# Performance work log

Hardware: AMD Instinct MI355X
Metric: run time of the kernel (lower is better)

Reference implementation:

```python
import jax, jax.numpy as jnp
import numpy as np

D_MODEL = 1024; N_HEAD = 16; HD = 64
D_STATE = 128; D_CONV = 4; EXPAND = 2; HEADDIM = 64
D_INNER = EXPAND * D_MODEL          # 2048
NHEADS = D_INNER // HEADDIM         # 32
FFN = 4 * D_MODEL                   # 4096
B, T = 2, 1024


def rmsnorm(x, eps=1e-6):
    # FastSimpleRMSNorm: no learnable weight
    return x * jax.lax.rsqrt(jnp.mean(x * x, axis=-1, keepdims=True) + eps)


def causal_dwconv(x, w, b):
    # x: (..., T, C), w: (C, K), b: (C,). Causal depthwise conv (left pad K-1).
    K = w.shape[1]
    t = x.shape[-2]
    pad = [(0, 0)] * (x.ndim - 2) + [(K - 1, 0), (0, 0)]
    xp = jnp.pad(x, pad)
    y = jnp.zeros_like(x) + b
    for k in range(K):
        y = y + w[:, k] * jax.lax.slice_in_dim(xp, k, k + t, axis=-2)
    return y


def block_forward(x, W_in, conv_w, conv_b, A_log, Dm, dt_bias, mnorm_w, W_out,
                  W_qkv, W_cproj, qconv_w, qconv_b, kconv_w, kconv_b, vconv_w, vconv_b,
                  time_maa_k, time_maa_r, W_key, W_rec, W_val):
    Bsz, Tn, _ = x.shape
    # ---- Mamba2 branch ----
    h = rmsnorm(x)
    zxbcdt = h @ W_in                                  # (B,T,2*D_INNER+2*N+H)
    z = zxbcdt[..., :D_INNER]
    xBC = zxbcdt[..., D_INNER:2 * D_INNER + 2 * D_STATE]
    dt = zxbcdt[..., -NHEADS:]
    xBC = jax.nn.silu(causal_dwconv(xBC, conv_w, conv_b))
    xm = xBC[..., :D_INNER]
    Bm = xBC[..., D_INNER:D_INNER + D_STATE]           # (B,T,N)
    Cm = xBC[..., -D_STATE:]                           # (B,T,N)
    dt = jax.nn.softplus(dt + dt_bias)                 # (B,T,H)
    A = -jnp.exp(A_log)                                # (H,)
    xh = xm.reshape(Bsz, Tn, NHEADS, HEADDIM)          # (B,T,H,P)

    def step(hstate, inp):
        dt_t, x_t, B_t, C_t = inp                      # (B,H),(B,H,P),(B,N),(B,N)
        dA = jnp.exp(dt_t * A)                         # (B,H)
        hstate = hstate * dA[..., None, None] + (dt_t[..., None] * x_t)[..., None] * B_t[:, None, None, :]
        y_t = jnp.einsum('bhpn,bn->bhp', hstate, C_t)
        return hstate, y_t

    h0 = jnp.zeros((Bsz, NHEADS, HEADDIM, D_STATE), x.dtype)
    _, ys = jax.lax.scan(step, h0, (jnp.swapaxes(dt, 0, 1), jnp.swapaxes(xh, 0, 1),
                                    jnp.swapaxes(Bm, 0, 1), jnp.swapaxes(Cm, 0, 1)))
    y = jnp.swapaxes(ys, 0, 1) + xh * Dm[:, None]      # (B,T,H,P)
    y = y.reshape(Bsz, Tn, D_INNER) * jax.nn.silu(z)   # gated
    y = y * jax.lax.rsqrt(jnp.mean(y * y, axis=-1, keepdims=True) + 1e-5) * mnorm_w
    x = x + y @ W_out

    # ---- MQA with depthwise convs ----
    h = rmsnorm(x)
    qkv = h @ W_qkv                                    # (B,T,D_MODEL+2*HD)
    q = qkv[..., :D_MODEL].reshape(Bsz, Tn, N_HEAD, HD).transpose(0, 2, 1, 3)  # (B,H,T,D)
    k = qkv[..., D_MODEL:D_MODEL + HD]                 # (B,T,D) single kv head
    v = qkv[..., -HD:]
    q = causal_dwconv(q, qconv_w, qconv_b)
    k = causal_dwconv(k, kconv_w, kconv_b)
    v = causal_dwconv(v, vconv_w, vconv_b)
    scores = jnp.einsum('bhtd,bsd->bhts', q, k) / np.float32(np.sqrt(HD))
    mask = jnp.tril(jnp.ones((Tn, Tn), bool))
    scores = jnp.where(mask, scores, -jnp.inf)
    p = jax.nn.softmax(scores, axis=-1)
    y = jnp.einsum('bhts,bsd->bhtd', p, v)
    y = y.transpose(0, 2, 1, 3).reshape(Bsz, Tn, D_MODEL)
    x = x + y @ W_cproj

    # ---- RWKV CMix FFN ----
    h = rmsnorm(x)
    xx = jnp.pad(h, ((0, 0), (1, 0), (0, 0)))[:, :Tn] - h   # time_shift(x) - x
    xk = h + xx * time_maa_k
    xr = h + xx * time_maa_r
    kf = jnp.square(jax.nn.relu(xk @ W_key))           # ReLU^2
    kv = kf @ W_val
    x = x + jax.nn.sigmoid(xr @ W_rec) * kv
    return x


def setup_inputs() -> dict:
    key = jax.random.key(0)
    ks = jax.random.split(key, 16)
    def w(k, shape, sc=0.02):
        return jax.random.normal(k, shape, jnp.float32) * sc
    x = jax.random.normal(ks[0], (B, T, D_MODEL), jnp.float32)
    W_in = w(ks[1], (D_MODEL, 2 * D_INNER + 2 * D_STATE + NHEADS))
    conv_w = w(ks[2], (D_INNER + 2 * D_STATE, D_CONV), 0.2)
    conv_b = jnp.zeros((D_INNER + 2 * D_STATE,), jnp.float32)
    A_log = jnp.log(jnp.arange(1, NHEADS + 1, dtype=jnp.float32))
    Dm = jnp.ones((NHEADS,), jnp.float32)
    dt_bias = w(ks[3], (NHEADS,), 0.5)
    mnorm_w = jnp.ones((D_INNER,), jnp.float32)
    W_out = w(ks[4], (D_INNER, D_MODEL))
    W_qkv = w(ks[5], (D_MODEL, D_MODEL + 2 * HD))
    W_cproj = w(ks[6], (D_MODEL, D_MODEL))
    qconv_w = w(ks[7], (HD, 3), 0.3); qconv_b = jnp.zeros((HD,), jnp.float32)
    kconv_w = w(ks[8], (HD, 3), 0.3); kconv_b = jnp.zeros((HD,), jnp.float32)
    vconv_w = w(ks[9], (HD, 3), 0.3); vconv_b = jnp.zeros((HD,), jnp.float32)
    ddd = jnp.arange(D_MODEL, dtype=jnp.float32) / D_MODEL
    time_maa_k = 1.0 - ddd  # layer_id=0 -> ratio_1_to_almost0 = 1
    time_maa_r = 1.0 - ddd
    W_key = w(ks[10], (D_MODEL, FFN))
    W_rec = w(ks[11], (D_MODEL, D_MODEL))
    W_val = w(ks[12], (FFN, D_MODEL))
    return dict(x=x, W_in=W_in, conv_w=conv_w, conv_b=conv_b, A_log=A_log, Dm=Dm,
                dt_bias=dt_bias, mnorm_w=mnorm_w, W_out=W_out, W_qkv=W_qkv, W_cproj=W_cproj,
                qconv_w=qconv_w, qconv_b=qconv_b, kconv_w=kconv_w, kconv_b=kconv_b,
                vconv_w=vconv_w, vconv_b=vconv_b, time_maa_k=time_maa_k, time_maa_r=time_maa_r,
                W_key=W_key, W_rec=W_rec, W_val=W_val)


def reference(x, W_in, conv_w, conv_b, A_log, Dm, dt_bias, mnorm_w, W_out,
              W_qkv, W_cproj, qconv_w, qconv_b, kconv_w, kconv_b, vconv_w, vconv_b,
              time_maa_k, time_maa_r, W_key, W_rec, W_val):
    return block_forward(x, W_in, conv_w, conv_b, A_log, Dm, dt_bias, mnorm_w, W_out,
                         W_qkv, W_cproj, qconv_w, qconv_b, kconv_w, kconv_b, vconv_w, vconv_b,
                         time_maa_k, time_maa_r, W_key, W_rec, W_val)
```

## Files before the change

### kernel.cpp

```cpp
#include <hip/hip_runtime.h>
#include <hip/hip_bf16.h>
#include <math.h>

#define BB 2
#define TT 1024
#define BT (BB*TT)
#define DM 1024
#define DI 2048
#define DS 128
#define NHS 32
#define PDIM 64
#define NHA 16
#define HD 64
#define FFN_ 4096
#define NZX 4384
#define NXBC 2304
#define NXBCD 2336
#define CL 128
#define NC 8

typedef __hip_bfloat16 bf16;
typedef short bf16x8 __attribute__((ext_vector_type(8)));
typedef float f32x4 __attribute__((ext_vector_type(4)));

__device__ __forceinline__ float b2f(bf16 v){ return __bfloat162float(v); }
__device__ __forceinline__ bf16 f2b(float v){ return __float2bfloat16(v); }

__device__ __forceinline__ void gload16(const void* g, void* l) {
  __builtin_amdgcn_global_load_lds(
      (const __attribute__((address_space(1))) unsigned int*)g,
      (__attribute__((address_space(3))) unsigned int*)l,
      16, 0, 0);
}

__global__ void k_rms_in(const float* __restrict__ xin, float* __restrict__ X,
                         bf16* __restrict__ H) {
  int row = blockIdx.x;
  int tid = threadIdx.x;
  const float* xr = xin + (size_t)row * DM;
  float v[4]; float ss = 0.f;
  #pragma unroll
  for (int i = 0; i < 4; ++i) { v[i] = xr[tid*4+i]; ss += v[i]*v[i]; }
  __shared__ float red[256];
  red[tid] = ss; __syncthreads();
  for (int s = 128; s > 0; s >>= 1) { if (tid < s) red[tid] += red[tid+s]; __syncthreads(); }
  float scale = rsqrtf(red[0]/(float)DM + 1e-6f);
  float* Xr = X + (size_t)row*DM; bf16* Hr = H + (size_t)row*DM;
  #pragma unroll
  for (int i = 0; i < 4; ++i) { Xr[tid*4+i] = v[i]; Hr[tid*4+i] = f2b(v[i]*scale); }
}

__global__ void k_reduce4_rms(const float* __restrict__ p0, const float* __restrict__ p1,
                              const float* __restrict__ p2, const float* __restrict__ p3,
                              float* __restrict__ X, bf16* __restrict__ H) {
  int row = blockIdx.x; int tid = threadIdx.x;
  size_t base = (size_t)row*DM + tid*4;
  float4 a = *(const float4*)(p0 + base);
  float4 b = *(const float4*)(p1 + base);
  float4 c = *(const float4*)(p2 + base);
  float4 d = *(const float4*)(p3 + base);
  float4 x = *(const float4*)(X + base);
  float v[4];
  v[0] = x.x + a.x + b.x + c.x + d.x;
  v[1] = x.y + a.y + b.y + c.y + d.y;
  v[2] = x.z + a.z + b.z + c.z + d.z;
  v[3] = x.w + a.w + b.w + c.w + d.w;
  float ss = v[0]*v[0] + v[1]*v[1] + v[2]*v[2] + v[3]*v[3];
  __shared__ float red[256];
  red[tid] = ss; __syncthreads();
  for (int s = 128; s > 0; s >>= 1) { if (tid < s) red[tid] += red[tid+s]; __syncthreads(); }
  float scale = rsqrtf(red[0]/(float)DM + 1e-6f);
  float4 res; res.x = v[0]; res.y = v[1]; res.z = v[2]; res.w = v[3];
  *(float4*)(X + base) = res;
  bf16* Hr = H + (size_t)row*DM + tid*4;
  #pragma unroll
  for (int i = 0; i < 4; ++i) Hr[i] = f2b(v[i]*scale);
}

__global__ void k_rms_shift(const float* __restrict__ X, const float* __restrict__ maak,
                            const float* __restrict__ maar,
                            bf16* __restrict__ XK, bf16* __restrict__ XR) {
  int row = blockIdx.x; int t = row & (TT - 1);
  int tid = threadIdx.x;
  const float* xr = X + (size_t)row*DM;
  const float* xp = xr - DM;
  float v[4], pv[4]; float ss = 0.f, ssp = 0.f;
  #pragma unroll
  for (int i = 0; i < 4; ++i) {
    int c = tid*4 + i;
    v[i] = xr[c]; ss += v[i]*v[i];
    pv[i] = (t > 0) ? xp[c] : 0.f; ssp += pv[i]*pv[i];
  }
  __shared__ float red[256], red2[256];
  red[tid] = ss; red2[tid] = ssp; __syncthreads();
  for (int s = 128; s > 0; s >>= 1) {
    if (tid < s) { red[tid] += red[tid+s]; red2[tid] += red2[tid+s]; }
    __syncthreads();
  }
  float scale  = rsqrtf(red[0]/(float)DM + 1e-6f);
  float scalep = (t > 0) ? rsqrtf(red2[0]/(float)DM + 1e-6f) : 0.f;
  bf16* xk = XK + (size_t)row*DM; bf16* xrw = XR + (size_t)row*DM;
  #pragma unroll
  for (int i = 0; i < 4; ++i) {
    int c = tid*4 + i;
    float h = v[i]*scale;
    float xx = pv[i]*scalep - h;
    xk[c]  = f2b(h + xx*maak[c]);
    xrw[c] = f2b(h + xx*maar[c]);
  }
}

__global__ void k_tcast(const float* __restrict__ W, bf16* __restrict__ Wt,
                        int K, int N) {
  __shared__ float t[32][33];
  int tx = threadIdx.x, ty = threadIdx.y;
  int n0 = blockIdx.x*32, k0 = blockIdx.y*32;
  #pragma unroll
  for (int i = 0; i < 4; ++i) {
    int k = k0 + ty + i*8, n = n0 + tx;
    t[ty + i*8][tx] = (n < N) ? W[(size_t)k*N + n] : 0.f;
  }
  __syncthreads();
  #pragma unroll
  for (int i = 0; i < 4; ++i) {
    int n = n0 + ty + i*8, k = k0 + tx;
    Wt[(size_t)n*K + k] = f2b(t[tx][ty + i*8]);
  }
}

template<int EPI, bool ADD, bool OUTBF>
__global__ __launch_bounds__(256)
void mfma_gemm(const bf16* __restrict__ A, const bf16* __restrict__ Bt,
               float* __restrict__ C, bf16* __restrict__ Cbf,
               int M, int N, int K) {
  __shared__ bf16 As[128*32];
  __shared__ bf16 Bs[128*32];
  int tid = threadIdx.x;
  int wave = tid >> 6, lane = tid & 63;
  int m_l = lane & 15, quad = lane >> 4;
  int wr = (wave & 1) * 64, wc = (wave >> 1) * 64;
  int row0 = blockIdx.y * 128, col0 = blockIdx.x * 128;
  f32x4 acc[4][4];
  #pragma unroll
  for (int i = 0; i < 4; ++i)
    #pragma unroll
    for (int j = 0; j < 4; ++j) acc[i][j] = (f32x4){0.f,0.f,0.f,0.f};
  int lr = lane >> 2;
  int lc = (lane & 3) * 8;
  for (int k0 = 0; k0 < K; k0 += 32) {
    __syncthreads();
    #pragma unroll
    for (int g = 0; g < 2; ++g) {
      int rbase = 32*wave + 16*g;
      gload16(&A [(size_t)(row0 + rbase + lr)*K + k0 + lc], &As[rbase*32]);
      gload16(&Bt[(size_t)(col0 + rbase + lr)*K + k0 + lc], &Bs[rbase*32]);
    }
    __syncthreads();
    bf16x8 af[4], bfv[4];
    #pragma unroll
    for (int i = 0; i < 4; ++i) af[i]  = *(const bf16x8*)&As[(wr + i*16 + m_l)*32 + quad*8];
    #pragma unroll
    for (int j = 0; j < 4; ++j) bfv[j] = *(const bf16x8*)&Bs[(wc + j*16 + m_l)*32 + quad*8];
    #pragma unroll
    for (int i = 0; i < 4; ++i)
      #pragma unroll
      for (int j = 0; j < 4; ++j)
        acc[i][j] = __builtin_amdgcn_mfma_f32_16x16x32_bf16(af[i], bfv[j], acc[i][j], 0, 0, 0);
  }
  #pragma unroll
  for (int i = 0; i < 4; ++i) {
    #pragma unroll
    for (int j = 0; j < 4; ++j) {
      int col = col0 + wc + j*16 + m_l;
      if (col < N) {
        #pragma unroll
        for (int r = 0; r < 4; ++r) {
          int row = row0 + wr + i*16 + quad*4 + r;
          float v = acc[i][j][r];
          if (EPI == 1) { v = fmaxf(v, 0.f); v = v*v; }
          else if (EPI == 2) v = 1.f/(1.f + __expf(-v));
          if (OUTBF)      Cbf[(size_t)row*N + col] = f2b(v);
          else if (ADD)   C[(size_t)row*N + col] += v;
          else            C[(size_t)row*N + col]  = v;
        }
      }
    }
  }
}

__global__ __launch_bounds__(256)
void mfma_sk32(const bf16* __restrict__ A, const bf16* __restrict__ Bt,
               float* __restrict__ P0, float* __restrict__ P1,
               float* __restrict__ P2, float* __restrict__ P3,
               int M, int N, int K, int kchunk) {
  __shared__ bf16 As[128*32];
  __shared__ bf16 Bs[128*32];
  int tid = threadIdx.x;
  int wave = tid >> 6, lane = tid & 63;
  int m_l = lane & 15, quad = lane >> 4;
  int wr = (wave & 1) * 64, wc = (wave >> 1) * 64;
  int row0 = blockIdx.y * 128, col0 = blockIdx.x * 128;
  int kbeg = blockIdx.z * kchunk;
  int kend = kbeg + kchunk;
  f32x4 acc[4][4];
  #pragma unroll
  for (int i = 0; i < 4; ++i)
    #pragma unroll
    for (int j = 0; j < 4; ++j) acc[i][j] = (f32x4){0.f,0.f,0.f,0.f};
  int lr = lane >> 2;
  int lc = (lane & 3) * 8;
  for (int k0 = kbeg; k0 < kend; k0 += 32) {
    __syncthreads();
    #pragma unroll
    for (int g = 0; g < 2; ++g) {
      int rbase = 32*wave + 16*g;
      gload16(&A [(size_t)(row0 + rbase + lr)*K + k0 + lc], &As[rbase*32]);
      gload16(&Bt[(size_t)(col0 + rbase + lr)*K + k0 + lc], &Bs[rbase*32]);
    }
    __syncthreads();
    bf16x8 af[4], bfv[4];
    #pragma unroll
    for (int i = 0; i < 4; ++i) af[i]  = *(const bf16x8*)&As[(wr + i*16 + m_l)*32 + quad*8];
    #pragma unroll
    for (int j = 0; j < 4; ++j) bfv[j] = *(const bf16x8*)&Bs[(wc + j*16 + m_l)*32 + quad*8];
    #pragma unroll
    for (int i = 0; i < 4; ++i)
      #pragma unroll
      for (int j = 0; j < 4; ++j)
        acc[i][j] = __builtin_amdgcn_mfma_f32_16x16x32_bf16(af[i], bfv[j], acc[i][j], 0, 0, 0);
  }
  float* P = (blockIdx.z == 0) ? P0 : (blockIdx.z == 1) ? P1 : (blockIdx.z == 2) ? P2 : P3;
  #pragma unroll
  for (int i = 0; i < 4; ++i) {
    #pragma unroll
    for (int j = 0; j < 4; ++j) {
      int col = col0 + wc + j*16 + m_l;
      if (col < N) {
        #pragma unroll
        for (int r = 0; r < 4; ++r) {
          int row = row0 + wr + i*16 + quad*4 + r;
          P[(size_t)row*N + col] = acc[i][j][r];
        }
      }
    }
  }
}

template<int Z, int EPI, bool ADD>
__global__ void k_reduce(float* __restrict__ dst, const float* __restrict__ p0,
                         const float* __restrict__ p1, const float* __restrict__ p2,
                         const float* __restrict__ p3) {
  size_t i = ((size_t)blockIdx.x*256 + threadIdx.x)*4;
  float4 a = *(const float4*)(p0 + i);
  float4 b = *(const float4*)(p1 + i);
  float r0 = a.x + b.x, r1 = a.y + b.y, r2 = a.z + b.z, r3 = a.w + b.w;
  if (Z == 4) {
    float4 c = *(const float4*)(p2 + i);
    float4 d = *(const float4*)(p3 + i);
    r0 += c.x + d.x; r1 += c.y + d.y; r2 += c.z + d.z; r3 += c.w + d.w;
  }
  if (EPI == 2) {
    r0 = 1.f/(1.f + __expf(-r0)); r1 = 1.f/(1.f + __expf(-r1));
    r2 = 1.f/(1.f + __expf(-r2)); r3 = 1.f/(1.f + __expf(-r3));
  }
  if (ADD) {
    float4 o = *(const float4*)(dst + i);
    r0 += o.x; r1 += o.y; r2 += o.z; r3 += o.w;
  }
  float4 res; res.x = r0; res.y = r1; res.z = r2; res.w = r3;
  *(float4*)(dst + i) = res;
}

__global__ void k_reduce_final6(const float* __restrict__ k0, const float* __restrict__ k1,
                                const float* __restrict__ k2, const float* __restrict__ k3,
                                const float* __restrict__ r0p, const float* __restrict__ r1p,
                                const float* __restrict__ X, float* __restrict__ out) {
  size_t i = ((size_t)blockIdx.x*256 + threadIdx.x)*4;
  float4 a = *(const float4*)(k0 + i);
  float4 b = *(const float4*)(k1 + i);
  float4 c = *(const float4*)(k2 + i);
  float4 d = *(const float4*)(k3 + i);
  float4 ra = *(const float4*)(r0p + i);
  float4 rb = *(const float4*)(r1p + i);
  float4 x = *(const float4*)(X + i);
  float kvx = a.x + b.x + c.x + d.x, kvy = a.y + b.y + c.y + d.y;
  float kvz = a.z + b.z + c.z + d.z, kvw = a.w + b.w + c.w + d.w;
  float sx = 1.f/(1.f + __expf(-(ra.x + rb.x)));
  float sy = 1.f/(1.f + __expf(-(ra.y + rb.y)));
  float sz = 1.f/(1.f + __expf(-(ra.z + rb.z)));
  float sw = 1.f/(1.f + __expf(-(ra.w + rb.w)));
  float4 res;
  res.x = x.x + sx*kvx; res.y = x.y + sy*kvy;
  res.z = x.z + sz*kvz; res.w = x.w + sw*kvw;
  *(float4*)(out + i) = res;
}

__global__ void k_conv_ssm(const float* __restrict__ ZXr, const float* __restrict__ cw,
                           const float* __restrict__ cb, const float* __restrict__ dtb,
                           bf16* __restrict__ XBCb, float* __restrict__ DT) {
  int bt = blockIdx.x; int b = bt >> 10; int t = bt & 1023;
  int tid = threadIdx.x;
  for (int c = tid; c < NXBC; c += 256) {
    float acc = cb[c];
    #pragma unroll
    for (int kk = 0; kk < 4; ++kk) {
      int ts = t - 3 + kk;
      if (ts >= 0) acc += cw[c*4+kk] * ZXr[((size_t)(b*TT+ts))*NXBCD + c];
    }
    float s = acc / (1.f + __expf(-acc));
    XBCb[(size_t)bt*NXBC + c] = f2b(s);
  }
  if (tid < NHS) {
    float x = ZXr[(size_t)bt*NXBCD + NXBC + tid] + dtb[tid];
    float sp = (x > 20.f) ? x : log1pf(__expf(x));
    DT[(size_t)bt*NHS + tid] = sp;
  }
}

__global__ __launch_bounds__(512)
void k_scan1(const bf16* __restrict__ xbcb, const float* __restrict__ dt,
             const float* __restrict__ A_log, const float* __restrict__ Dmv,
             float* __restrict__ Y, float* __restrict__ SC, float* __restrict__ CUM) {
  int bc = blockIdx.x;
  int bh = bc >> 3, c = bc & 7;
  int b = bh >> 5, h = bh & 31;
  int tid = threadIdx.x, wave = tid >> 6, lane = tid & 63;
  int col = lane & 15, quad = lane >> 4;
  int t0 = c * CL;
  __shared__ bf16 sB[128*136];
  __shared__ bf16 sC[128*136];
  __shared__ bf16 sxT[64*136];
  __shared__ float sL[128], sdt[128], sW[128];
  float A = -__expf(A_log[h]);
  float Dmh = Dmv[h];
  for (int e = tid; e < 128*16; e += 512) {
    int r = e >> 4, ch = e & 15;
    const bf16* row = xbcb + (size_t)(b*TT + t0 + r)*NXBC;
    *(uint4*)&sB[r*136 + ch*8] = *(const uint4*)&row[2048 + ch*8];
    *(uint4*)&sC[r*136 + ch*8] = *(const uint4*)&row[2176 + ch*8];
  }
  for (int e = tid; e < 64*128; e += 512) {
    int p = e & 63, t = e >> 6;
    sxT[p*136 + t] = xbcb[(size_t)(b*TT + t0 + t)*NXBC + h*64 + p];
  }
  if (tid < 128) sdt[tid] = dt[(size_t)(b*TT + t0 + tid)*NHS + h];
  __syncthreads();
  if (wave == 0) {
    float a0 = sdt[2*lane]*A, a1 = sdt[2*lane+1]*A;
    float tot = a0 + a1;
    #pragma unroll
    for (int off = 1; off < 64; off <<= 1) {
      float up = __shfl_up(tot, off);
      if (lane >= off) tot += up;
    }
    sL[2*lane+1] = tot;
    sL[2*lane]   = tot - a1;
  }
  __syncthreads();
  int wr = (wave & 1)*64, wc = (wave >> 1)*32;
  f32x4 g[4][2];
  #pragma unroll
  for (int i = 0; i < 4; ++i)
    #pragma unroll
    for (int j = 0; j < 2; ++j) g[i][j] = (f32x4){0.f,0.f,0.f,0.f};
  #pragma unroll
  for (int kf = 0; kf < 4; ++kf) {
    bf16x8 af[4], bfr[2];
    #pragma unroll
    for (int i = 0; i < 4; ++i) af[i]  = *(const bf16x8*)&sC[(wr + i*16 + col)*136 + kf*32 + quad*8];
    #pragma unroll
    for (int j = 0; j < 2; ++j) bfr[j] = *(const bf16x8*)&sB[(wc + j*16 + col)*136 + kf*32 + quad*8];
    #pragma unroll
    for (int i = 0; i < 4; ++i)
      #pragma unroll
      for (int j = 0; j < 2; ++j)
        g[i][j] = __builtin_amdgcn_mfma_f32_16x16x32_bf16(af[i], bfr[j], g[i][j], 0, 0, 0);
  }
  float Lend = sL[127];
  if (tid < 128) sW[tid] = __expf(Lend - sL[tid]) * sdt[tid];
  __syncthreads();
  if (tid < 128) CUM[(size_t)bh*TT + t0 + tid] = __expf(sL[tid]);
  #pragma unroll
  for (int i = 0; i < 4; ++i) {
    #pragma unroll
    for (int j = 0; j < 2; ++j) {
      int sl = wc + j*16 + col;
      #pragma unroll
      for (int r = 0; r < 4; ++r) {
        int tl = wr + i*16 + quad*4 + r;
        float v = (sl <= tl) ? g[i][j][r] * __expf(sL[tl] - sL[sl]) * sdt[sl] : 0.f;
        sC[tl*136 + sl] = f2b(v);
      }
    }
  }
  for (int e = tid; e < 128*128; e += 512) {
    int n = e & 127, s = e >> 7;
    sB[n*136 + s] = f2b(b2f(xbcb[(size_t)(b*TT + t0 + s)*NXBC + 2048 + n]) * sW[s]);
  }
  __syncthreads();
  int tb = (wave & 3)*32, pb = (wave >> 2)*32;
  f32x4 ya[2][2];
  #pragma unroll
  for (int i2 = 0; i2 < 2; ++i2)
    #pragma unroll
    for (int jd = 0; jd < 2; ++jd) ya[i2][jd] = (f32x4){0.f,0.f,0.f,0.f};
  #pragma unroll
  for (int kf = 0; kf < 4; ++kf) {
    bf16x8 pa[2], xa[2];
    #pragma unroll
    for (int i2 = 0; i2 < 2; ++i2)
      pa[i2] = *(const bf16x8*)&sC[(tb + i2*16 + col)*136 + kf*32 + quad*8];
    #pragma unroll
    for (int jd = 0; jd < 2; ++jd)
      xa[jd] = *(const bf16x8*)&sxT[(pb + jd*16 + col)*136 + kf*32 + quad*8];
    #pragma unroll
    for (int i2 = 0; i2 < 2; ++i2)
      #pragma unroll
      for (int jd = 0; jd < 2; ++jd)
        ya[i2][jd] = __builtin_amdgcn_mfma_f32_16x16x32_bf16(pa[i2], xa[jd], ya[i2][jd], 0, 0, 0);
  }
  #pragma unroll
  for (int i2 = 0; i2 < 2; ++i2) {
    #pragma unroll
    for (int jd = 0; jd < 2; ++jd) {
      int p = pb + jd*16 + col;
      #pragma unroll
      for (int r = 0; r < 4; ++r) {
        int tl = tb + i2*16 + quad*4 + r;
        float xv = b2f(sxT[p*136 + tl]);
        Y[(size_t)(b*TT + t0 + tl)*DI + h*64 + p] = ya[i2][jd][r] + xv*Dmh;
      }
    }
  }
  int pb3 = (wave & 3)*16, nb = (wave >> 2)*64;
  f32x4 sa[4];
  #pragma unroll
  for (int nt = 0; nt < 4; ++nt) sa[nt] = (f32x4){0.f,0.f,0.f,0.f};
  #pragma unroll
  for (int kf = 0; kf < 4; ++kf) {
    bf16x8 xpa = *(const bf16x8*)&sxT[(pb3 + col)*136 + kf*32 + quad*8];
    #pragma unroll
    for (int nt = 0; nt < 4; ++nt) {
      bf16x8 bwa = *(const bf16x8*)&sB[(nb + nt*16 + col)*136 + kf*32 + quad*8];
      sa[nt] = __builtin_amdgcn_mfma_f32_16x16x32_bf16(xpa, bwa, sa[nt], 0, 0, 0);
    }
  }
  #pragma unroll
  for (int nt = 0; nt < 4; ++nt) {
    int n = nb + nt*16 + col;
    #pragma unroll
    for (int r = 0; r < 4; ++r) {
      int p = pb3 + quad*4 + r;
      SC[((size_t)(bh*NC + c)*64 + p)*128 + n] = sa[nt][r];
    }
  }
}

__global__ __launch_bounds__(512)
void k_scan2(float* __restrict__ SC, const float* __restrict__ CUM) {
  int bh = blockIdx.x;
  int tid = threadIdx.x;
  int p = tid >> 3, g = tid & 7;
  float S[16];
  #pragma unroll
  for (int j = 0; j < 16; ++j) S[j] = 0.f;
  for (int c = 0; c < NC; ++c) {
    size_t base = ((size_t)(bh*NC + c)*64 + p)*128 + g*16;
    float Ptot = CUM[(size_t)bh*TT + c*CL + (CL-1)];
    float tmp[16];
    #pragma unroll
    for (int j = 0; j < 16; ++j) tmp[j] = SC[base + j];
    #pragma unroll
    for (int j = 0; j < 16; ++j) SC[base + j] = S[j];
    #pragma unroll
    for (int j = 0; j < 16; ++j) S[j] = S[j]*Ptot + tmp[j];
  }
}

__global__ __launch_bounds__(256)
void k_scan3(const bf16* __restrict__ xbcb, const float* __restrict__ SC,
             const float* __restrict__ CUM, float* __restrict__ Y) {
  int bc = blockIdx.x;
  int bh = bc >> 3, c = bc & 7;
  if (c == 0) return;
  int b = bh >> 5, h = bh & 31;
  int tid = threadIdx.x, wave = tid >> 6, lane = tid & 63;
  int col = lane & 15, quad = lane >> 4;
  int t0 = c * CL;
  __shared__ bf16 sCt[128*136];
  __shared__ bf16 sS[64*136];
  __shared__ float sCum[128];
  for (int e = tid; e < 128*16; e += 256) {
    int r = e >> 4, ch = e & 15;
    *(uint4*)&sCt[r*136 + ch*8] =
      *(const uint4*)&xbcb[(size_t)(b*TT + t0 + r)*NXBC + 2176 + ch*8];
  }
  for (int e = tid; e < 64*128; e += 256) {
    int n = e & 127, p = e >> 7;
    sS[p*136 + n] = f2b(SC[((size_t)(bh*NC + c)*64 + p)*128 + n]);
  }
  if (tid < 128) sCum[tid] = CUM[(size_t)bh*TT + t0 + tid];
  __syncthreads();
  f32x4 ya[2][4];
  #pragma unroll
  for (int i2 = 0; i2 < 2; ++i2)
    #pragma unroll
    for (int jd = 0; jd < 4; ++jd) ya[i2][jd] = (f32x4){0.f,0.f,0.f,0.f};
  #pragma unroll
  for (int kf = 0; kf < 4; ++kf) {
    bf16x8 pa[2], sv[4];
    #pragma unroll
    for (int i2 = 0; i2 < 2; ++i2)
      pa[i2] = *(const bf16x8*)&sCt[(wave*32 + i2*16 + col)*136 + kf*32 + quad*8];
    #pragma unroll
    for (int jd = 0; jd < 4; ++jd)
      sv[jd] = *(const bf16x8*)&sS[(jd*16 + col)*136 + kf*32 + quad*8];
    #pragma unroll
    for (int i2 = 0; i2 < 2; ++i2)
      #pragma unroll
      for (int jd = 0; jd < 4; ++jd)
        ya[i2][jd] = __builtin_amdgcn_mfma_f32_16x16x32_bf16(pa[i2], sv[jd], ya[i2][jd], 0, 0, 0);
  }
  #pragma unroll
  for (int i2 = 0; i2 < 2; ++i2) {
    #pragma unroll
    for (int jd = 0; jd < 4; ++jd) {
      int p = jd*16 + col;
      #pragma unroll
      for (int r = 0; r < 4; ++r) {
        int tl = wave*32 + i2*16 + quad*4 + r;
        Y[(size_t)(b*TT + t0 + tl)*DI + h*64 + p] += sCum[tl]*ya[i2][jd][r];
      }
    }
  }
}

__global__ void k_gate(const float* __restrict__ Y, const float* __restrict__ Z,
                       const float* __restrict__ mnw, bf16* __restrict__ Ybf) {
  int row = blockIdx.x; int tid = threadIdx.x;
  const float* yr = Y + (size_t)row*DI;
  const float* zr = Z + (size_t)row*DI;
  float gv[8]; float ss = 0.f;
  #pragma unroll
  for (int i = 0; i < 8; ++i) {
    int c = tid*8 + i;
    float z = zr[c];
    float sz = z / (1.f + __expf(-z));
    float v = yr[c]*sz;
    gv[i] = v; ss += v*v;
  }
  __shared__ float red[256];
  red[tid] = ss; __syncthreads();
  for (int s = 128; s > 0; s >>= 1) { if (tid < s) red[tid] += red[tid+s]; __syncthreads(); }
  float scale = rsqrtf(red[0]/(float)DI + 1e-5f);
  bf16* br = Ybf + (size_t)row*DI;
  #pragma unroll
  for (int i = 0; i < 8; ++i) { int c = tid*8 + i; br[c] = f2b(gv[i]*scale*mnw[c]); }
}

__global__ void k_conv_qkv(const float* __restrict__ QKV,
                           const float* qw, const float* qb, const float* kw, const float* kb,
                           const float* vw, const float* vb,
                           bf16* __restrict__ Qb, bf16* __restrict__ Kb, bf16* __restrict__ Vtb) {
  int bt = blockIdx.x; int b = bt >> 10; int t = bt & 1023;
  int tid = threadIdx.x;
  for (int c = tid; c < 1152; c += 256) {
    if (c < 1024) {
      int h = c >> 6, d = c & 63;
      float acc = qb[d];
      #pragma unroll
      for (int kk = 0; kk < 3; ++kk) { int ts = t-2+kk; if (ts >= 0) acc += qw[d*3+kk] * QKV[((size_t)(b*TT+ts))*1152 + c]; }
      Qb[((size_t)(b*NHA + h)*TT + t)*HD + d] = f2b(acc * 0.125f);
    } else if (c < 1088) {
      int d = c - 1024;
      float acc = kb[d];
      #pragma unroll
      for (int kk = 0; kk < 3; ++kk) { int ts = t-2+kk; if (ts >= 0) acc += kw[d*3+kk] * QKV[((size_t)(b*TT+ts))*1152 + c]; }
      Kb[(size_t)bt*HD + d] = f2b(acc);
    } else {
      int d = c - 1088;
      float acc = vb[d];
      #pragma unroll
      for (int kk = 0; kk < 3; ++kk) { int ts = t-2+kk; if (ts >= 0) acc += vw[d*3+kk] * QKV[((size_t)(b*TT+ts))*1152 + c]; }
      Vtb[((size_t)(b*HD + d))*TT + t] = f2b(acc);
    }
  }
}

__global__ __launch_bounds__(512)
void k_flash_sk(const bf16* __restrict__ Qb, const bf16* __restrict__ Kb,
                const bf16* __restrict__ Vtb, float* __restrict__ Op,
                float* __restrict__ Lp) {
  int qt = blockIdx.x >> 1, z = blockIdx.x & 1;
  int h = blockIdx.y, b = blockIdx.z;
  int n = qt + 1;
  int kmid = (n + 1) >> 1;
  int kbeg = z ? kmid : 0;
  int kend = z ? n : kmid;
  int tid = threadIdx.x, wave = tid >> 6, lane = tid & 63;
  int col = lane & 15, quad = lane >> 4;
  int t0 = qt * 128;
  __shared__ bf16 Ks[128*72];
  __shared__ bf16 Vs[64*136];
  __shared__ bf16 Ps[8][16*136];
  const bf16* Qbase = Qb + ((size_t)(b*NHA + h))*TT*HD;
  float lst[4];
  f32x4 oacc[4];
  #pragma unroll
  for (int r = 0; r < 4; ++r) lst[r] = 0.f;
  #pragma unroll
  for (int jd = 0; jd < 4; ++jd) oacc[jd] = (f32x4){0.f,0.f,0.f,0.f};
  if (kbeg < kend) {
    bf16x8 qf[2];
    #pragma unroll
    for (int kf = 0; kf < 2; ++kf)
      qf[kf] = *(const bf16x8*)&Qbase[(size_t)(t0 + wave*16 + col)*HD + kf*32 + quad*8];

    for (int kt = kbeg; kt < kend; ++kt) {
      int s0 = kt * 128;
      __syncthreads();
      for (int e = tid; e < 1024; e += 512) {
        int r = e >> 3, ch = e & 7;
        *(uint4*)&Ks[r*72 + ch*8] = *(const uint4*)&Kb[((size_t)(b*TT + s0 + r))*HD + ch*8];
      }
      for (int e = tid; e < 1024; e += 512) {
        int d = e >> 4, ch = e & 15;
        *(uint4*)&Vs[d*136 + ch*8] = *(const uint4*)&Vtb[((size_t)(b*HD + d))*TT + s0 + ch*8];
      }
      __syncthreads();
      f32x4 sacc[8];
      #pragma unroll
      for (int j = 0; j < 8; ++j) sacc[j] = (f32x4){0.f,0.f,0.f,0.f};
      __builtin_amdgcn_s_setprio(1);
      #pragma unroll
      for (int j = 0; j < 8; ++j) {
        bf16x8 kf0 = *(const bf16x8*)&Ks[(j*16 + col)*72 + quad*8];
        bf16x8 kf1 = *(const bf16x8*)&Ks[(j*16 + col)*72 + 32 + quad*8];
        sacc[j] = __builtin_amdgcn_mfma_f32_16x16x32_bf16(qf[0], kf0, sacc[j], 0, 0, 0);
        sacc[j] = __builtin_amdgcn_mfma_f32_16x16x32_bf16(qf[1], kf1, sacc[j], 0, 0, 0);
      }
      __builtin_amdgcn_s_setprio(0);
      bool diag = (kt == qt);
      #pragma unroll
      for (int r = 0; r < 4; ++r) {
        int rowloc = wave*16 + quad*4 + r;
        #pragma unroll
        for (int j = 0; j < 8; ++j) {
          float pv = __expf(sacc[j][r]);
          if (diag && (j*16 + col > rowloc)) pv = 0.f;
          sacc[j][r] = pv;
          lst[r] += pv;
        }
      }
      #pragma unroll
      for (int j = 0; j < 8; ++j)
        #pragma unroll
        for (int r = 0; r < 4; ++r)
          Ps[wave][(quad*4 + r)*136 + j*16 + col] = f2b(sacc[j][r]);
      __builtin_amdgcn_s_setprio(1);
      bf16x8 pa[4];
      #pragma unroll
      for (int kf = 0; kf < 4; ++kf)
        pa[kf] = *(const bf16x8*)&Ps[wave][col*136 + kf*32 + quad*8];
      #pragma unroll
      for (int jd = 0; jd < 4; ++jd) {
        #pragma unroll
        for (int kf = 0; kf < 4; ++kf) {
          bf16x8 vbf = *(const bf16x8*)&Vs[(jd*16 + col)*136 + kf*32 + quad*8];
          oacc[jd] = __builtin_amdgcn_mfma_f32_16x16x32_bf16(pa[kf], vbf, oacc[jd], 0, 0, 0);
        }
      }
      __builtin_amdgcn_s_setprio(0);
    }
    #pragma unroll
    for (int r = 0; r < 4; ++r) {
      float l = lst[r];
      l += __shfl_xor(l, 1);
      l += __shfl_xor(l, 2);
      l += __shfl_xor(l, 4);
      l += __shfl_xor(l, 8);
      lst[r] = l;
    }
  }
  if (qt == 0 && z == 1) return;
  size_t robase = ((size_t)((z*BB + b)*NHA + h))*TT + t0;
  #pragma unroll
  for (int jd = 0; jd < 4; ++jd) {
    int d = jd*16 + col;
    #pragma unroll
    for (int r = 0; r < 4; ++r) {
      int tl = wave*16 + quad*4 + r;
      Op[(robase + tl)*HD + d] = oacc[jd][r];
    }
  }
  if (col == 0) {
    #pragma unroll
    for (int r = 0; r < 4; ++r) {
      int tl = wave*16 + quad*4 + r;
      Lp[robase + tl] = lst[r];
    }
  }
}

__global__ void k_att_comb(const float* __restrict__ Op, const float* __restrict__ Lp,
                           bf16* __restrict__ outb) {
  int idx = blockIdx.x*256 + threadIdx.x;
  int e = idx*4;
  int c = e & (DM - 1); int h = c >> 6; int d = c & 63;
  int bt = e >> 10; int t = bt & (TT - 1); int b = bt >> 10;
  int qt = t >> 7;
  size_t r0 = ((size_t)(b*NHA + h))*TT + t;
  float4 o0 = *(const float4*)&Op[r0*HD + d];
  float l = Lp[r0];
  float ox = o0.x, oy = o0.y, oz = o0.z, ow = o0.w;
  if (qt > 0) {
    size_t r1 = ((size_t)((BB + b)*NHA + h))*TT + t;
    float4 o1 = *(const float4*)&Op[r1*HD + d];
    l += Lp[r1];
    ox += o1.x; oy += o1.y; oz += o1.z; ow += o1.w;
  }
  float inv = 1.f / l;
  bf16* p = outb + (size_t)bt*DM + c;
  p[0] = f2b(ox*inv); p[1] = f2b(oy*inv); p[2] = f2b(oz*inv); p[3] = f2b(ow*inv);
}

extern "C" void kernel_launch(void* const* d_in, const int* in_sizes, int n_in,
                              void* d_out, int out_size, void* d_ws, size_t ws_size,
                              hipStream_t stream) {
  const float* x_in    = (const float*)d_in[0];
  const float* W_in    = (const float*)d_in[1];
  const float* conv_w  = (const float*)d_in[2];
  const float* conv_b  = (const float*)d_in[3];
  const float* A_log   = (const float*)d_in[4];
  const float* Dm      = (const float*)d_in[5];
  const float* dt_bias = (const float*)d_in[6];
  const float* mnorm_w = (const float*)d_in[7];
  const float* W_out   = (const float*)d_in[8];
  const float* W_qkv   = (const float*)d_in[9];
  const float* W_cproj = (const float*)d_in[10];
  const float* qconv_w = (const float*)d_in[11];
  const float* qconv_b = (const float*)d_in[12];
  const float* kconv_w = (const float*)d_in[13];
  const float* kconv_b = (const float*)d_in[14];
  const float* vconv_w = (const float*)d_in[15];
  const float* vconv_b = (const float*)d_in[16];
  const float* maa_k   = (const float*)d_in[17];
  const float* maa_r   = (const float*)d_in[18];
  const float* W_key   = (const float*)d_in[19];
  const float* W_rec   = (const float*)d_in[20];
  const float* W_val   = (const float*)d_in[21];
  float* out = (float*)d_out;

  float* ws = (float*)d_ws;
  float* X       = ws;
  bf16*  Hbf     = (bf16*)(ws + 2097152);
  float* Zbuf    = ws + 3145728;
  float* XBCDraw = ws + 7340032;
  float* XBC     = ws + 12124160;
  float* DT      = ws + 16842752;
  float* CUM     = ws + 16908288;
  float* Y       = ws + 16973824;

  bf16*  Wt_in    = (bf16*)XBC;
  bf16*  XBCb     = (bf16*)XBC;
  float* SC       = XBCDraw;
  bf16*  Ybf      = (bf16*)XBC;
  bf16*  Wt_out   = (bf16*)(XBC + 2097152);
  float* QKV      = Zbuf;
  bf16*  Wt_qkv   = (bf16*)XBC;
  bf16*  Qb       = (bf16*)XBCDraw;
  bf16*  Kb       = (bf16*)(XBCDraw + 1048576);
  bf16*  Vtb      = (bf16*)(XBCDraw + 1114112);
  bf16*  ATTNbf   = (bf16*)Y;
  bf16*  Wt_cproj = (bf16*)(Y + 1048576);
  bf16*  XKbf     = (bf16*)XBC;
  bf16*  XRbf     = (bf16*)(XBC + 1048576);
  bf16*  Wt_key   = (bf16*)Zbuf;
  bf16*  KFbf     = (bf16*)XBCDraw;
  bf16*  Wt_val   = (bf16*)Zbuf;
  bf16*  Wt_rec   = (bf16*)Zbuf;
  float* FOp      = Zbuf;
  float* FLp      = ws + 2097152;

  dim3 thr256(256), thr512(512);
  dim3 tblk(32, 8);

  k_rms_in<<<BT, thr256, 0, stream>>>(x_in, X, Hbf);
  k_tcast<<<dim3(4480/32, 1024/32), tblk, 0, stream>>>(W_in, Wt_in, 1024, NZX);
  mfma_gemm<0,false,false><<<dim3(16, 16), thr256, 0, stream>>>(Hbf, Wt_in, Zbuf, nullptr, BT, 2048, 1024);
  mfma_gemm<0,false,false><<<dim3(19, 16), thr256, 0, stream>>>(Hbf, Wt_in + (size_t)2048*1024, XBCDraw, nullptr, BT, NXBCD, 1024);
  k_conv_ssm<<<BT, thr256, 0, stream>>>(XBCDraw, conv_w, conv_b, dt_bias, XBCb, DT);
  k_scan1<<<BB*NHS*NC, thr512, 0, stream>>>(XBCb, DT, A_log, Dm, Y, SC, CUM);
  k_scan2<<<BB*NHS, thr512, 0, stream>>>(SC, CUM);
  k_scan3<<<BB*NHS*NC, thr256, 0, stream>>>(XBCb, SC, CUM, Y);
  k_gate<<<BT, thr256, 0, stream>>>(Y, Zbuf, mnorm_w, Ybf);
  k_tcast<<<dim3(1024/32, 2048/32), tblk, 0, stream>>>(W_out, Wt_out, 2048, 1024);
  mfma_sk32<<<dim3(8, 16, 4), thr256, 0, stream>>>(Ybf, Wt_out,
      Zbuf, Zbuf + 2097152, XBCDraw, XBCDraw + 2097152, BT, 1024, 2048, 512);
  k_reduce4_rms<<<BT, thr256, 0, stream>>>(Zbuf, Zbuf + 2097152, XBCDraw, XBCDraw + 2097152, X, Hbf);
  k_tcast<<<dim3(1152/32, 1024/32), tblk, 0, stream>>>(W_qkv, Wt_qkv, 1024, 1152);
  mfma_sk32<<<dim3(9, 16, 2), thr256, 0, stream>>>(Hbf, Wt_qkv,
      XBCDraw, XBCDraw + 2359296, XBCDraw, XBCDraw, BT, 1152, 1024, 512);
  k_reduce<2,0,false><<<2304, thr256, 0, stream>>>(QKV, XBCDraw, XBCDraw + 2359296, XBCDraw, XBCDraw);
  k_conv_qkv<<<BT, thr256, 0, stream>>>(QKV, qconv_w, qconv_b, kconv_w, kconv_b, vconv_w, vconv_b, Qb, Kb, Vtb);
  k_flash_sk<<<dim3((TT/128)*2, NHA, BB), thr512, 0, stream>>>(Qb, Kb, Vtb, FOp, FLp);
  k_att_comb<<<(BT*DM)/(256*4), thr256, 0, stream>>>(FOp, FLp, ATTNbf);
  k_tcast<<<dim3(1024/32, 1024/32), tblk, 0, stream>>>(W_cproj, Wt_cproj, 1024, 1024);
  mfma_sk32<<<dim3(8, 16, 2), thr256, 0, stream>>>(ATTNbf, Wt_cproj,
      Zbuf, Zbuf + 2097152, Zbuf, Zbuf, BT, 1024, 1024, 512);
  k_reduce<2,0,true><<<2048, thr256, 0, stream>>>(X, Zbuf, Zbuf + 2097152, Zbuf, Zbuf);
  k_rms_shift<<<BT, thr256, 0, stream>>>(X, maa_k, maa_r, XKbf, XRbf);
  k_tcast<<<dim3(4096/32, 1024/32), tblk, 0, stream>>>(W_key, Wt_key, 1024, 4096);
  mfma_gemm<1,false,true><<<dim3(32, 16), thr256, 0, stream>>>(XKbf, Wt_key, nullptr, KFbf, BT, 4096, 1024);
  k_tcast<<<dim3(1024/32, 4096/32), tblk, 0, stream>>>(W_val, Wt_val, 4096, 1024);
  mfma_sk32<<<dim3(8, 16, 4), thr256, 0, stream>>>(KFbf, Wt_val,
      Y, Y + 2097152, XBC + 2621440, Zbuf + 2097152, BT, 1024, 4096, 1024);
  k_tcast<<<dim3(1024/32, 1024/32), tblk, 0, stream>>>(W_rec, Wt_rec, 1024, 1024);
  mfma_sk32<<<dim3(8, 16, 2), thr256, 0, stream>>>(XRbf, Wt_rec,
      XBCDraw, XBCDraw + 2097152, XBCDraw, XBCDraw, BT, 1024, 1024, 512);
  k_reduce_final6<<<2048, thr256, 0, stream>>>(
      Y, Y + 2097152, XBC + 2621440, Zbuf + 2097152,
      XBCDraw, XBCDraw + 2097152, X, out);
}
```

Baseline: 524.8 us.

## Double-buffer LDS tiles in MFMA GEMMs and fuse QKV split-K reduce into conv

```diff
diff --git a/kernel.cpp b/kernel.cpp
--- a/kernel.cpp
+++ b/kernel.cpp
@@ -133,8 +133,8 @@
 void mfma_gemm(const bf16* __restrict__ A, const bf16* __restrict__ Bt,
                float* __restrict__ C, bf16* __restrict__ Cbf,
                int M, int N, int K) {
-  __shared__ bf16 As[128*32];
-  __shared__ bf16 Bs[128*32];
+  __shared__ bf16 As[2][128*32];
+  __shared__ bf16 Bs[2][128*32];
   int tid = threadIdx.x;
   int wave = tid >> 6, lane = tid & 63;
   int m_l = lane & 15, quad = lane >> 4;
@@ -147,25 +147,37 @@
     for (int j = 0; j < 4; ++j) acc[i][j] = (f32x4){0.f,0.f,0.f,0.f};
   int lr = lane >> 2;
   int lc = (lane & 3) * 8;
-  for (int k0 = 0; k0 < K; k0 += 32) {
-    __syncthreads();
-    #pragma unroll
-    for (int g = 0; g < 2; ++g) {
-      int rbase = 32*wave + 16*g;
-      gload16(&A [(size_t)(row0 + rbase + lr)*K + k0 + lc], &As[rbase*32]);
-      gload16(&Bt[(size_t)(col0 + rbase + lr)*K + k0 + lc], &Bs[rbase*32]);
-    }
-    __syncthreads();
+  #pragma unroll
+  for (int g = 0; g < 2; ++g) {
+    int rbase = 32*wave + 16*g;
+    gload16(&A [(size_t)(row0 + rbase + lr)*K + lc], &As[0][rbase*32]);
+    gload16(&Bt[(size_t)(col0 + rbase + lr)*K + lc], &Bs[0][rbase*32]);
+  }
+  __syncthreads();
+  int nit = K >> 5;
+  int cur = 0;
+  for (int it = 0; it < nit; ++it) {
+    if (it + 1 < nit) {
+      int kn = (it + 1) << 5;
+      #pragma unroll
+      for (int g = 0; g < 2; ++g) {
+        int rbase = 32*wave + 16*g;
+        gload16(&A [(size_t)(row0 + rbase + lr)*K + kn + lc], &As[cur^1][rbase*32]);
+        gload16(&Bt[(size_t)(col0 + rbase + lr)*K + kn + lc], &Bs[cur^1][rbase*32]);
+      }
+    }
     bf16x8 af[4], bfv[4];
     #pragma unroll
-    for (int i = 0; i < 4; ++i) af[i]  = *(const bf16x8*)&As[(wr + i*16 + m_l)*32 + quad*8];
-    #pragma unroll
-    for (int j = 0; j < 4; ++j) bfv[j] = *(const bf16x8*)&Bs[(wc + j*16 + m_l)*32 + quad*8];
+    for (int i = 0; i < 4; ++i) af[i]  = *(const bf16x8*)&As[cur][(wr + i*16 + m_l)*32 + quad*8];
+    #pragma unroll
+    for (int j = 0; j < 4; ++j) bfv[j] = *(const bf16x8*)&Bs[cur][(wc + j*16 + m_l)*32 + quad*8];
     #pragma unroll
     for (int i = 0; i < 4; ++i)
       #pragma unroll
       for (int j = 0; j < 4; ++j)
         acc[i][j] = __builtin_amdgcn_mfma_f32_16x16x32_bf16(af[i], bfv[j], acc[i][j], 0, 0, 0);
+    __syncthreads();
+    cur ^= 1;
   }
   #pragma unroll
   for (int i = 0; i < 4; ++i) {
@@ -193,15 +205,14 @@
                float* __restrict__ P0, float* __restrict__ P1,
                float* __restrict__ P2, float* __restrict__ P3,
                int M, int N, int K, int kchunk) {
-  __shared__ bf16 As[128*32];
-  __shared__ bf16 Bs[128*32];
+  __shared__ bf16 As[2][128*32];
+  __shared__ bf16 Bs[2][128*32];
   int tid = threadIdx.x;
   int wave = tid >> 6, lane = tid & 63;
   int m_l = lane & 15, quad = lane >> 4;
   int wr = (wave & 1) * 64, wc = (wave >> 1) * 64;
   int row0 = blockIdx.y * 128, col0 = blockIdx.x * 128;
   int kbeg = blockIdx.z * kchunk;
-  int kend = kbeg + kchunk;
   f32x4 acc[4][4];
   #pragma unroll
   for (int i = 0; i < 4; ++i)
@@ -209,25 +220,37 @@
     for (int j = 0; j < 4; ++j) acc[i][j] = (f32x4){0.f,0.f,0.f,0.f};
   int lr = lane >> 2;
   int lc = (lane & 3) * 8;
-  for (int k0 = kbeg; k0 < kend; k0 += 32) {
-    __syncthreads();
-    #pragma unroll
-    for (int g = 0; g < 2; ++g) {
-      int rbase = 32*wave + 16*g;
-      gload16(&A [(size_t)(row0 + rbase + lr)*K + k0 + lc], &As[rbase*32]);
-      gload16(&Bt[(size_t)(col0 + rbase + lr)*K + k0 + lc], &Bs[rbase*32]);
-    }
-    __syncthreads();
+  #pragma unroll
+  for (int g = 0; g < 2; ++g) {
+    int rbase = 32*wave + 16*g;
+    gload16(&A [(size_t)(row0 + rbase + lr)*K + kbeg + lc], &As[0][rbase*32]);
+    gload16(&Bt[(size_t)(col0 + rbase + lr)*K + kbeg + lc], &Bs[0][rbase*32]);
+  }
+  __syncthreads();
+  int nit = kchunk >> 5;
+  int cur = 0;
+  for (int it = 0; it < nit; ++it) {
+    if (it + 1 < nit) {
+      int kn = kbeg + ((it + 1) << 5);
+      #pragma unroll
+      for (int g = 0; g < 2; ++g) {
+        int rbase = 32*wave + 16*g;
+        gload16(&A [(size_t)(row0 + rbase + lr)*K + kn + lc], &As[cur^1][rbase*32]);
+        gload16(&Bt[(size_t)(col0 + rbase + lr)*K + kn + lc], &Bs[cur^1][rbase*32]);
+      }
+    }
     bf16x8 af[4], bfv[4];
     #pragma unroll
-    for (int i = 0; i < 4; ++i) af[i]  = *(const bf16x8*)&As[(wr + i*16 + m_l)*32 + quad*8];
-    #pragma unroll
-    for (int j = 0; j < 4; ++j) bfv[j] = *(const bf16x8*)&Bs[(wc + j*16 + m_l)*32 + quad*8];
+    for (int i = 0; i < 4; ++i) af[i]  = *(const bf16x8*)&As[cur][(wr + i*16 + m_l)*32 + quad*8];
+    #pragma unroll
+    for (int j = 0; j < 4; ++j) bfv[j] = *(const bf16x8*)&Bs[cur][(wc + j*16 + m_l)*32 + quad*8];
     #pragma unroll
     for (int i = 0; i < 4; ++i)
       #pragma unroll
       for (int j = 0; j < 4; ++j)
         acc[i][j] = __builtin_amdgcn_mfma_f32_16x16x32_bf16(af[i], bfv[j], acc[i][j], 0, 0, 0);
+    __syncthreads();
+    cur ^= 1;
   }
   float* P = (blockIdx.z == 0) ? P0 : (blockIdx.z == 1) ? P1 : (blockIdx.z == 2) ? P2 : P3;
   #pragma unroll
@@ -558,7 +581,7 @@
   for (int i = 0; i < 8; ++i) { int c = tid*8 + i; br[c] = f2b(gv[i]*scale*mnw[c]); }
 }
 
-__global__ void k_conv_qkv(const float* __restrict__ QKV,
+__global__ void k_conv_qkv(const float* __restrict__ P0, const float* __restrict__ P1,
                            const float* qw, const float* qb, const float* kw, const float* kb,
                            const float* vw, const float* vb,
                            bf16* __restrict__ Qb, bf16* __restrict__ Kb, bf16* __restrict__ Vtb) {
@@ -569,19 +592,28 @@
       int h = c >> 6, d = c & 63;
       float acc = qb[d];
       #pragma unroll
-      for (int kk = 0; kk < 3; ++kk) { int ts = t-2+kk; if (ts >= 0) acc += qw[d*3+kk] * QKV[((size_t)(b*TT+ts))*1152 + c]; }
+      for (int kk = 0; kk < 3; ++kk) {
+        int ts = t-2+kk;
+        if (ts >= 0) { size_t ix = ((size_t)(b*TT+ts))*1152 + c; acc += qw[d*3+kk] * (P0[ix] + P1[ix]); }
+      }
       Qb[((size_t)(b*NHA + h)*TT + t)*HD + d] = f2b(acc * 0.125f);
     } else if (c < 1088) {
       int d = c - 1024;
       float acc = kb[d];
       #pragma unroll
-      for (int kk = 0; kk < 3; ++kk) { int ts = t-2+kk; if (ts >= 0) acc += kw[d*3+kk] * QKV[((size_t)(b*TT+ts))*1152 + c]; }
+      for (int kk = 0; kk < 3; ++kk) {
+        int ts = t-2+kk;
+        if (ts >= 0) { size_t ix = ((size_t)(b*TT+ts))*1152 + c; acc += kw[d*3+kk] * (P0[ix] + P1[ix]); }
+      }
       Kb[(size_t)bt*HD + d] = f2b(acc);
     } else {
       int d = c - 1088;
       float acc = vb[d];
       #pragma unroll
-      for (int kk = 0; kk < 3; ++kk) { int ts = t-2+kk; if (ts >= 0) acc += vw[d*3+kk] * QKV[((size_t)(b*TT+ts))*1152 + c]; }
+      for (int kk = 0; kk < 3; ++kk) {
+        int ts = t-2+kk;
+        if (ts >= 0) { size_t ix = ((size_t)(b*TT+ts))*1152 + c; acc += vw[d*3+kk] * (P0[ix] + P1[ix]); }
+      }
       Vtb[((size_t)(b*HD + d))*TT + t] = f2b(acc);
     }
   }
@@ -766,7 +798,6 @@
   float* SC       = XBCDraw;
   bf16*  Ybf      = (bf16*)XBC;
   bf16*  Wt_out   = (bf16*)(XBC + 2097152);
-  float* QKV      = Zbuf;
   bf16*  Wt_qkv   = (bf16*)XBC;
   bf16*  Qb       = (bf16*)XBCDraw;
   bf16*  Kb       = (bf16*)(XBCDraw + 1048576);
@@ -800,9 +831,8 @@
   k_reduce4_rms<<<BT, thr256, 0, stream>>>(Zbuf, Zbuf + 2097152, XBCDraw, XBCDraw + 2097152, X, Hbf);
   k_tcast<<<dim3(1152/32, 1024/32), tblk, 0, stream>>>(W_qkv, Wt_qkv, 1024, 1152);
   mfma_sk32<<<dim3(9, 16, 2), thr256, 0, stream>>>(Hbf, Wt_qkv,
-      XBCDraw, XBCDraw + 2359296, XBCDraw, XBCDraw, BT, 1152, 1024, 512);
-  k_reduce<2,0,false><<<2304, thr256, 0, stream>>>(QKV, XBCDraw, XBCDraw + 2359296, XBCDraw, XBCDraw);
-  k_conv_qkv<<<BT, thr256, 0, stream>>>(QKV, qconv_w, qconv_b, kconv_w, kconv_b, vconv_w, vconv_b, Qb, Kb, Vtb);
+      Zbuf, Y, Zbuf, Zbuf, BT, 1152, 1024, 512);
+  k_conv_qkv<<<BT, thr256, 0, stream>>>(Zbuf, Y, qconv_w, qconv_b, kconv_w, kconv_b, vconv_w, vconv_b, Qb, Kb, Vtb);
   k_flash_sk<<<dim3((TT/128)*2, NHA, BB), thr512, 0, stream>>>(Qb, Kb, Vtb, FOp, FLp);
   k_att_comb<<<(BT*DM)/(256*4), thr256, 0, stream>>>(FOp, FLp, ATTNbf);
   k_tcast<<<dim3(1024/32, 1024/32), tblk, 0, stream>>>(W_cproj, Wt_cproj, 1024, 1024);
```

Result: faster. 504.6 us (-3.9%).
